# Performance work log

Measured on AMD Instinct MI355X. Metric: run time of the kernel, lower is better.

Reference implementation:

```python
import jax, jax.numpy as jnp
import numpy as np

B, S, D, H, FF, L, U = 64, 256, 128, 8, 512, 4, 5000
N, E, FEA, HW, CED, TD = 40000, 160000, 32, 16, 16, 6
DH = D // H


def _ln(x, g, b):
    m = jnp.mean(x, -1, keepdims=True)
    v = jnp.var(x, -1, keepdims=True)
    return (x - m) * jax.lax.rsqrt(v + 1e-5) * g + b


def _sin_pe(s, d):
    pos = jnp.arange(s, dtype=jnp.float32)[:, None]
    div = jnp.exp(jnp.arange(0, d, 2, dtype=jnp.float32) * (-np.log(10000.0) / d))
    ang = pos * div  # [S, D/2]
    return jnp.stack([jnp.sin(ang), jnp.cos(ang)], -1).reshape(s, d)


def setup_inputs() -> dict:
    key = jax.random.key(0)
    ks = jax.random.split(key, 40)
    sc = 0.02
    inp = {}
    inp['node_feature'] = jax.random.normal(ks[0], (N, FEA), jnp.float32)
    inp['edge_index'] = jax.random.randint(ks[1], (2, E), 0, N)
    inp['traj_x'] = jax.random.randint(ks[2], (B, S), 0, N)
    inp['temporal_x'] = jax.random.normal(ks[3], (B, S, TD), jnp.float32)
    inp['user_id_x'] = jax.random.randint(ks[4], (B, 1), 0, U)
    inp['mask'] = jnp.ones((B, S), jnp.int32)
    inp['end_idx'] = jax.random.randint(ks[5], (B,), 0, S)
    inp['idx_without_end'] = jax.random.randint(ks[6], (B,), 0, S)
    inp['temporal_mat_x'] = jax.random.uniform(ks[7], (B, S, S), jnp.float32) * 3600.0
    inp['dis_mat_x'] = jax.random.uniform(ks[8], (B, S, S), jnp.float32) * 5000.0
    inp['highway_x'] = jax.random.randint(ks[9], (B, S), 0, HW)
    inp['lambda2'] = jnp.float32(0.5)
    # --- learned parameters ---
    inp['gnn_w1'] = jax.random.normal(ks[10], (FEA, D), jnp.float32) * sc
    inp['gnn_b1'] = jnp.zeros((D,), jnp.float32)
    inp['gnn_w2'] = jax.random.normal(ks[11], (D, D), jnp.float32) * sc
    inp['gnn_b2'] = jnp.zeros((D,), jnp.float32)
    inp['ue_tab'] = jax.random.normal(ks[12], (U, D), jnp.float32) * sc
    inp['ce_tab'] = jax.random.normal(ks[13], (HW, CED), jnp.float32) * sc
    inp['fl_w'] = jax.random.normal(ks[14], (TD + CED, D), jnp.float32) * sc
    inp['fl_b'] = jnp.zeros((D,), jnp.float32)
    inp['wqkv'] = jax.random.normal(ks[15], (L, D, 3 * D), jnp.float32) * sc
    inp['bqkv'] = jnp.zeros((L, 3 * D), jnp.float32)
    inp['wo'] = jax.random.normal(ks[16], (L, D, D), jnp.float32) * sc
    inp['bo'] = jnp.zeros((L, D), jnp.float32)
    inp['ln1_g'] = jnp.ones((L, D), jnp.float32)
    inp['ln1_b'] = jnp.zeros((L, D), jnp.float32)
    inp['ln2_g'] = jnp.ones((L, D), jnp.float32)
    inp['ln2_b'] = jnp.zeros((L, D), jnp.float32)
    inp['ffn_w1'] = jax.random.normal(ks[17], (L, D, FF), jnp.float32) * sc
    inp['ffn_b1'] = jnp.zeros((L, FF), jnp.float32)
    inp['ffn_w2'] = jax.random.normal(ks[18], (L, FF, D), jnp.float32) * sc
    inp['ffn_b2'] = jnp.zeros((L, D), jnp.float32)
    inp['head_w'] = jax.random.normal(ks[19], (D, U), jnp.float32) * sc
    inp['head_b'] = jnp.zeros((U,), jnp.float32)
    return inp


def reference(node_feature, edge_index, traj_x, temporal_x, user_id_x, mask,
              end_idx, idx_without_end, temporal_mat_x, dis_mat_x, highway_x,
              lambda2,
              gnn_w1, gnn_b1, gnn_w2, gnn_b2, ue_tab, ce_tab, fl_w, fl_b,
              wqkv, bqkv, wo, bo, ln1_g, ln1_b, ln2_g, ln2_b,
              ffn_w1, ffn_b1, ffn_w2, ffn_b2, head_w, head_b):
    # --- spatial (road-network) GNN encoder: spe ---
    src, dst = edge_index[0], edge_index[1]
    deg = jax.ops.segment_sum(jnp.ones((E,), jnp.float32), dst, num_segments=N)
    h = node_feature
    for W, b in ((gnn_w1, gnn_b1), (gnn_w2, gnn_b2)):
        agg = jax.ops.segment_sum(h[src], dst, num_segments=N) / (deg[:, None] + 1.0)
        h = jax.nn.relu((h + agg) @ W + b)
    spe = h  # [N, D]
    # --- embedding fusion ---
    ce = ce_tab[highway_x]                                  # [B,S,CED]
    ue = ue_tab[user_id_x]                                  # [B,1,D] broadcast
    fuse = jax.nn.relu(jnp.concatenate([temporal_x, ce], -1) @ fl_w + fl_b)
    x = spe[traj_x] + ue + fuse                             # [B,S,D]
    x = x + _sin_pe(S, D)[None]
    # --- relative temporal/distance attention bias ---
    rel = lambda2 * jnp.log1p(temporal_mat_x) + (1.0 - lambda2) * jnp.log1p(dis_mat_x)
    mbias = jnp.where(mask[:, None, None, :] > 0, 0.0, -1e9)
    bias = mbias - rel[:, None]                             # [B,1,S,S]
    scale = 1.0 / float(np.sqrt(DH))
    for l in range(L):
        qkv = x @ wqkv[l] + bqkv[l]
        q, k, v = jnp.split(qkv, 3, axis=-1)
        q = q.reshape(B, S, H, DH).transpose(0, 2, 1, 3)
        k = k.reshape(B, S, H, DH).transpose(0, 2, 1, 3)
        v = v.reshape(B, S, H, DH).transpose(0, 2, 1, 3)
        scores = jnp.einsum('bhqd,bhkd->bhqk', q, k) * scale + bias
        a = jax.nn.softmax(scores, -1)
        o = jnp.einsum('bhqk,bhkd->bhqd', a, v).transpose(0, 2, 1, 3).reshape(B, S, D)
        x = _ln(x + o @ wo[l] + bo[l], ln1_g[l], ln1_b[l])
        f = jax.nn.relu(x @ ffn_w1[l] + ffn_b1[l]) @ ffn_w2[l] + ffn_b2[l]
        x = _ln(x + f, ln2_g[l], ln2_b[l])
    # --- gather last token + classifier head ---
    traj_emb = x[jnp.arange(B), end_idx]                    # [B,D]
    return traj_emb @ head_w + head_b                       # [B,U]
```

## Files before the change

kernel.cpp:

```cpp
#include <hip/hip_runtime.h>
#include <hip/hip_fp16.h>
#include <cstdint>
#include <cstddef>

typedef unsigned short u16;
typedef __attribute__((ext_vector_type(8))) short short8;
typedef __attribute__((ext_vector_type(4))) float f32x4;

#define B_   64
#define S_   256
#define D_   128
#define H_   8
#define DH_  16
#define FF_  512
#define L_   4
#define U_   5000
#define UP_  5120
#define N_   40000
#define NP_  40064
#define E_   160000
#define FEA_ 32
#define HWY_ 16
#define CED_ 16
#define TD_  6
#define NSCB 157
#define UB_CNT_END 160
#define UB_CVT_END 1592
#define UB_TOTAL   5688

static __device__ __forceinline__ u16 f2b(float f) {
    unsigned int u = __float_as_uint(f);
    unsigned int r = (u + 0x7FFFu + ((u >> 16) & 1u)) >> 16;
    return (u16)r;
}
static __device__ __forceinline__ float b2f(u16 u) {
    return __uint_as_float(((unsigned int)u) << 16);
}
static __device__ __forceinline__ u16 f2h(float f) {
    return __half_as_ushort(__float2half(f));
}
static __device__ __forceinline__ float h2f(u16 u) {
    return __half2float(__ushort_as_half(u));
}

static __device__ __forceinline__ void gload16(const void* g, void* l) {
    __builtin_amdgcn_global_load_lds(
        (const __attribute__((address_space(1))) unsigned int*)g,
        (__attribute__((address_space(3))) unsigned int*)l,
        16, 0, 0);
}

struct UberArgs {
    const float* csrc[7];
    u16* cdst[7];
    int K[7], Npad[7], Nsrc[7], Kp[7], base[7];
    const float* tm; const float* dm; const int* maskp; const float* lambda2;
    u16* bias; int* cnt;
};

__global__ __launch_bounds__(256) void k_uber(UberArgs a) {
    __shared__ float tile[32][33];
    int bid = blockIdx.x, tid = threadIdx.x;
    if (bid < UB_CNT_END) {
        int idx = bid * 256 + tid;
        if (idx < NP_) a.cnt[idx] = 0;
        return;
    }
    if (bid < UB_CVT_END) {
        int t = 0;
#pragma unroll
        for (int i = 1; i < 7; ++i) t += (bid >= a.base[i]);
        int rb = bid - a.base[t];
        int K = a.K[t], Npad = a.Npad[t], Nsrc = a.Nsrc[t], Kp = a.Kp[t];
        int nbn = Npad >> 5, nbk = Kp >> 5;
        int per = nbn * nbk;
        int l = rb / per, rem = rb - l * per;
        int n0 = (rem % nbn) * 32, k0 = (rem / nbn) * 32;
        const float* in = a.csrc[t];
        u16* outp = a.cdst[t];
        int j = tid & 31, i2 = tid >> 5;
#pragma unroll
        for (int r = 0; r < 4; ++r) {
            int k = k0 + i2 + r * 8, n = n0 + j;
            tile[i2 + r * 8][j] = (k < K && n < Nsrc) ? in[(size_t)l * K * Nsrc + (size_t)k * Nsrc + n] : 0.f;
        }
        __syncthreads();
#pragma unroll
        for (int r = 0; r < 4; ++r) {
            int n = n0 + i2 + r * 8, k = k0 + j;
            if (n < Npad && k < Kp)
                outp[(size_t)l * Npad * Kp + (size_t)n * Kp + k] = f2b(tile[j][i2 + r * 8]);
        }
        return;
    }
    int t4 = (bid - UB_CVT_END) * 256 + tid;
    const int total = B_ * S_ * S_ / 4;
    if (t4 >= total) return;
    float l2 = *a.lambda2, l2c = 1.f - l2;
    float4 av = ((const float4*)a.tm)[t4];
    float4 bv = ((const float4*)a.dm)[t4];
    int basei = t4 * 4;
    int bb = basei >> 16;
    int k0 = basei & 255;
    const int* mrow = a.maskp + bb * S_;
    float r0 = (mrow[k0 + 0] > 0 ? 0.f : -30000.f) - (l2 * __logf(1.f + av.x) + l2c * __logf(1.f + bv.x));
    float r1 = (mrow[k0 + 1] > 0 ? 0.f : -30000.f) - (l2 * __logf(1.f + av.y) + l2c * __logf(1.f + bv.y));
    float r2 = (mrow[k0 + 2] > 0 ? 0.f : -30000.f) - (l2 * __logf(1.f + av.z) + l2c * __logf(1.f + bv.z));
    float r3 = (mrow[k0 + 3] > 0 ? 0.f : -30000.f) - (l2 * __logf(1.f + av.w) + l2c * __logf(1.f + bv.w));
    *(ushort4*)&a.bias[(size_t)t4 * 4] = make_ushort4(f2h(r0), f2h(r1), f2h(r2), f2h(r3));
}

__global__ __launch_bounds__(256) void k_count(const int* __restrict__ dst, int* __restrict__ cnt) {
    int e = blockIdx.x * 256 + threadIdx.x;
    if (e < E_) atomicAdd(&cnt[dst[e]], 1);
}

__global__ __launch_bounds__(256) void k_scanA(const int* __restrict__ cnt, int* __restrict__ part) {
    __shared__ int sh[256];
    int idx = blockIdx.x * 256 + threadIdx.x;
    sh[threadIdx.x] = (idx < NP_) ? cnt[idx] : 0;
    __syncthreads();
    for (int o = 128; o > 0; o >>= 1) {
        if (threadIdx.x < o) sh[threadIdx.x] += sh[threadIdx.x + o];
        __syncthreads();
    }
    if (threadIdx.x == 0) part[blockIdx.x] = sh[0];
}

__global__ __launch_bounds__(256) void k_scanB(const int* __restrict__ cnt, const int* __restrict__ part,
                                               int* __restrict__ off, int* __restrict__ cursor) {
    __shared__ int sh[256];
    __shared__ int bsum;
    int tid = threadIdx.x;
    int pv = (tid < blockIdx.x) ? part[tid] : 0;
    sh[tid] = pv;
    __syncthreads();
    for (int o = 128; o > 0; o >>= 1) {
        if (tid < o) sh[tid] += sh[tid + o];
        __syncthreads();
    }
    if (tid == 0) bsum = sh[0];
    __syncthreads();
    int basev = bsum;
    __syncthreads();
    int idx = blockIdx.x * 256 + tid;
    int v = (idx < NP_) ? cnt[idx] : 0;
    sh[tid] = v;
    __syncthreads();
    for (int o = 1; o < 256; o <<= 1) {
        int t2 = (tid >= o) ? sh[tid - o] : 0;
        __syncthreads();
        sh[tid] += t2;
        __syncthreads();
    }
    if (idx < NP_) {
        int res = sh[tid] - v + basev;
        off[idx] = res;
        cursor[idx] = res;
    }
}

__global__ __launch_bounds__(256) void k_fill(const int* __restrict__ src, const int* __restrict__ dst,
                                              int* __restrict__ cursor, int* __restrict__ ebuf) {
    int e = blockIdx.x * 256 + threadIdx.x;
    if (e >= E_) return;
    int p = atomicAdd(&cursor[dst[e]], 1);
    ebuf[p] = src[e];
}

__global__ __launch_bounds__(256) void k_gprep1(const float* __restrict__ nf, const int* __restrict__ off,
                                                const int* __restrict__ cnt, const int* __restrict__ ebuf,
                                                u16* __restrict__ out) {
    int n = blockIdx.x * 8 + (threadIdx.x >> 5);
    int f = threadIdx.x & 31;
    u16 r = 0;
    if (n < N_) {
        int start = off[n], c = cnt[n];
        float acc = 0.f;
        int i = 0;
        for (; i + 4 <= c; i += 4) {
            int s0 = ebuf[start + i], s1 = ebuf[start + i + 1];
            int s2 = ebuf[start + i + 2], s3 = ebuf[start + i + 3];
            float v0 = nf[(size_t)s0 * FEA_ + f];
            float v1 = nf[(size_t)s1 * FEA_ + f];
            float v2 = nf[(size_t)s2 * FEA_ + f];
            float v3 = nf[(size_t)s3 * FEA_ + f];
            acc += (v0 + v1) + (v2 + v3);
        }
        for (; i < c; ++i) {
            int s = ebuf[start + i];
            acc += nf[(size_t)s * FEA_ + f];
        }
        r = f2b(nf[(size_t)n * FEA_ + f] + acc / (float)(c + 1));
    }
    if (n < NP_) {
        out[(size_t)n * 64 + f] = r;
        out[(size_t)n * 64 + 32 + f] = 0;
    }
}

__global__ __launch_bounds__(256) void k_gprep2(const u16* __restrict__ h1b, const int* __restrict__ off,
                                                const int* __restrict__ cnt, const int* __restrict__ ebuf,
                                                u16* __restrict__ out) {
    int n = blockIdx.x * 4 + (threadIdx.x >> 6);
    int d2 = (threadIdx.x & 63) * 2;
    if (n >= NP_) return;
    u16 r0 = 0, r1 = 0;
    if (n < N_) {
        int start = off[n], c = cnt[n];
        float a0 = 0.f, a1 = 0.f;
        int i = 0;
        for (; i + 4 <= c; i += 4) {
            int s0 = ebuf[start + i], s1 = ebuf[start + i + 1];
            int s2 = ebuf[start + i + 2], s3 = ebuf[start + i + 3];
            ushort2 v0 = *(const ushort2*)&h1b[(size_t)s0 * D_ + d2];
            ushort2 v1 = *(const ushort2*)&h1b[(size_t)s1 * D_ + d2];
            ushort2 v2 = *(const ushort2*)&h1b[(size_t)s2 * D_ + d2];
            ushort2 v3 = *(const ushort2*)&h1b[(size_t)s3 * D_ + d2];
            a0 += (b2f(v0.x) + b2f(v1.x)) + (b2f(v2.x) + b2f(v3.x));
            a1 += (b2f(v0.y) + b2f(v1.y)) + (b2f(v2.y) + b2f(v3.y));
        }
        for (; i < c; ++i) {
            int s = ebuf[start + i];
            ushort2 v = *(const ushort2*)&h1b[(size_t)s * D_ + d2];
            a0 += b2f(v.x); a1 += b2f(v.y);
        }
        float rinv = 1.f / (float)(c + 1);
        ushort2 sv = *(const ushort2*)&h1b[(size_t)n * D_ + d2];
        r0 = f2b(b2f(sv.x) + a0 * rinv);
        r1 = f2b(b2f(sv.y) + a1 * rinv);
    }
    *(ushort2*)&out[(size_t)n * D_ + d2] = make_ushort2(r0, r1);
}

template<int BM, int ACT, int OUTB, int RES, int LN, int GAT>
__global__ __launch_bounds__(256) void k_mgemm(const u16* __restrict__ A, const u16* __restrict__ BT,
                                               const float* __restrict__ bias, const float* __restrict__ resid,
                                               void* __restrict__ Cout,
                                               const float* __restrict__ g, const float* __restrict__ be,
                                               u16* __restrict__ xbout, const int* __restrict__ endi,
                                               int M, int N, int K) {
    constexpr int SMEMB = (BM == 128) ? (LN ? 128 * 133 * 4 : 32768)
                                      : (LN ? 64 * 133 * 4 : 24576);
    __shared__ __align__(16) char smem[SMEMB];
    u16* Al = (u16*)smem;
    u16* Bl = Al + (BM == 128 ? 128 * 64 : 64 * 64);
    int tid = threadIdx.x;
    int wid = tid >> 6, lane = tid & 63;
    int row0 = blockIdx.x * BM;
    int col0 = blockIdx.y * 128;
    f32x4 acc[4][4] = {};
    int rA = lane & 15, kq = lane >> 4;

    for (int k0 = 0; k0 < K; k0 += 64) {
        if (k0) __syncthreads();
        if (BM == 128) {
            int srow = wid * 32 + (lane >> 3);
            int ks8 = ((lane & 7) ^ (lane >> 3)) * 8;
#pragma unroll
            for (int i = 0; i < 4; ++i) {
                int row = srow + i * 8;
                size_t arow = (size_t)(row0 + row);
                if (GAT) {
                    int bb2 = row0 + row;
                    arow = (bb2 < B_) ? ((size_t)bb2 * S_ + endi[bb2]) : 0;
                }
                gload16(A + arow * K + k0 + ks8, &Al[(wid * 32 + i * 8) * 64]);
                gload16(BT + (size_t)(col0 + row) * K + k0 + ks8, &Bl[(wid * 32 + i * 8) * 64]);
            }
        } else {
#pragma unroll
            for (int i = 0; i < 6; ++i) {
                int c = wid * 6 + i;
                int rr = c * 8 + (lane >> 3);
                int sl = (((lane & 7) ^ (rr & 7)) << 3);
                if (c < 8) {
                    size_t arow = (size_t)(row0 + rr);
                    if (GAT) {
                        int bb2 = row0 + rr;
                        arow = (bb2 < B_) ? ((size_t)bb2 * S_ + endi[bb2]) : 0;
                    }
                    gload16(A + arow * K + k0 + sl, &Al[rr * 64]);
                } else {
                    gload16(BT + (size_t)(col0 + rr - 64) * K + k0 + sl, &Bl[(rr - 64) * 64]);
                }
            }
        }
        __syncthreads();
#pragma unroll
        for (int ks = 0; ks < 2; ++ks) {
            int sw = ((ks * 4 + kq) ^ (rA & 7)) * 8;
            if (BM == 128) {
                int wr = wid >> 1, wc = wid & 1;
                short8 af[4], bfr[4];
#pragma unroll
                for (int m = 0; m < 4; ++m)
                    af[m] = *(const short8*)&Al[(64 * wr + m * 16 + rA) * 64 + sw];
#pragma unroll
                for (int n = 0; n < 4; ++n)
                    bfr[n] = *(const short8*)&Bl[(64 * wc + n * 16 + rA) * 64 + sw];
#pragma unroll
                for (int m = 0; m < 4; ++m)
#pragma unroll
                    for (int n = 0; n < 4; ++n)
                        acc[m][n] = __builtin_amdgcn_mfma_f32_16x16x32_bf16(af[m], bfr[n], acc[m][n], 0, 0, 0);
            } else {
                int wr2 = wid & 1, wc2 = wid >> 1;
                short8 af[2], bfr[4];
#pragma unroll
                for (int m = 0; m < 2; ++m)
                    af[m] = *(const short8*)&Al[(wr2 * 32 + m * 16 + rA) * 64 + sw];
#pragma unroll
                for (int n = 0; n < 4; ++n)
                    bfr[n] = *(const short8*)&Bl[(wc2 * 64 + n * 16 + rA) * 64 + sw];
#pragma unroll
                for (int m = 0; m < 2; ++m)
#pragma unroll
                    for (int n = 0; n < 4; ++n)
                        acc[m][n] = __builtin_amdgcn_mfma_f32_16x16x32_bf16(af[m], bfr[n], acc[m][n], 0, 0, 0);
            }
        }
    }

    if (LN) {
        float* vbuf = (float*)smem;
        __syncthreads();
        constexpr int MR = (BM == 128) ? 4 : 2;
#pragma unroll
        for (int m = 0; m < MR; ++m) {
#pragma unroll
            for (int n = 0; n < 4; ++n) {
                int cc, rl0;
                if (BM == 128) { cc = (wid & 1) * 64 + n * 16 + rA; rl0 = (wid >> 1) * 64 + m * 16 + kq * 4; }
                else           { cc = (wid >> 1) * 64 + n * 16 + rA; rl0 = (wid & 1) * 32 + m * 16 + kq * 4; }
                float bv = bias[cc];
#pragma unroll
                for (int r = 0; r < 4; ++r) {
                    int rl = rl0 + r;
                    float v = acc[m][n][r] + bv + resid[(size_t)(row0 + rl) * 128 + cc];
                    vbuf[rl * 133 + cc] = v;
                }
            }
        }
        __syncthreads();
        if (BM == 128) {
            int rl = tid >> 1, half = tid & 1;
            const float* vrow = vbuf + rl * 133 + half * 64;
            float4 vv[16];
            float s = 0.f, s2 = 0.f;
#pragma unroll
            for (int j = 0; j < 16; ++j) {
                vv[j] = *(const float4*)(vrow + j * 4);
                s += (vv[j].x + vv[j].y) + (vv[j].z + vv[j].w);
                s2 += (vv[j].x * vv[j].x + vv[j].y * vv[j].y) + (vv[j].z * vv[j].z + vv[j].w * vv[j].w);
            }
            s += __shfl_xor(s, 1, 64);
            s2 += __shfl_xor(s2, 1, 64);
            float mean = s * (1.f / 128.f);
            float var = s2 * (1.f / 128.f) - mean * mean;
            float rs = rsqrtf(var + 1e-5f);
            int grow = row0 + rl;
            float* xrow = (float*)Cout + (size_t)grow * 128 + half * 64;
            u16* xbrow = xbout + (size_t)grow * 128 + half * 64;
#pragma unroll
            for (int j = 0; j < 16; ++j) {
                float4 gv = *(const float4*)(g + half * 64 + j * 4);
                float4 bv = *(const float4*)(be + half * 64 + j * 4);
                float o0 = (vv[j].x - mean) * rs * gv.x + bv.x;
                float o1 = (vv[j].y - mean) * rs * gv.y + bv.y;
                float o2 = (vv[j].z - mean) * rs * gv.z + bv.z;
                float o3 = (vv[j].w - mean) * rs * gv.w + bv.w;
                *(float4*)(xrow + j * 4) = make_float4(o0, o1, o2, o3);
                *(ushort4*)(xbrow + j * 4) = make_ushort4(f2b(o0), f2b(o1), f2b(o2), f2b(o3));
            }
        } else {
            int rl = tid >> 2, q4 = tid & 3;
            const float* vrow = vbuf + rl * 133 + q4 * 32;
            float4 vv[8];
            float s = 0.f, s2 = 0.f;
#pragma unroll
            for (int j = 0; j < 8; ++j) {
                vv[j] = *(const float4*)(vrow + j * 4);
                s += (vv[j].x + vv[j].y) + (vv[j].z + vv[j].w);
                s2 += (vv[j].x * vv[j].x + vv[j].y * vv[j].y) + (vv[j].z * vv[j].z + vv[j].w * vv[j].w);
            }
            s += __shfl_xor(s, 1, 64);  s2 += __shfl_xor(s2, 1, 64);
            s += __shfl_xor(s, 2, 64);  s2 += __shfl_xor(s2, 2, 64);
            float mean = s * (1.f / 128.f);
            float var = s2 * (1.f / 128.f) - mean * mean;
            float rs = rsqrtf(var + 1e-5f);
            int grow = row0 + rl;
            float* xrow = (float*)Cout + (size_t)grow * 128 + q4 * 32;
            u16* xbrow = xbout + (size_t)grow * 128 + q4 * 32;
#pragma unroll
            for (int j = 0; j < 8; ++j) {
                float4 gv = *(const float4*)(g + q4 * 32 + j * 4);
                float4 bv = *(const float4*)(be + q4 * 32 + j * 4);
                float o0 = (vv[j].x - mean) * rs * gv.x + bv.x;
                float o1 = (vv[j].y - mean) * rs * gv.y + bv.y;
                float o2 = (vv[j].z - mean) * rs * gv.z + bv.z;
                float o3 = (vv[j].w - mean) * rs * gv.w + bv.w;
                *(float4*)(xrow + j * 4) = make_float4(o0, o1, o2, o3);
                *(ushort4*)(xbrow + j * 4) = make_ushort4(f2b(o0), f2b(o1), f2b(o2), f2b(o3));
            }
        }
    } else {
        constexpr int MR = (BM == 128) ? 4 : 2;
#pragma unroll
        for (int m = 0; m < MR; ++m) {
#pragma unroll
            for (int n = 0; n < 4; ++n) {
                int cc, cr0;
                if (BM == 128) { cc = col0 + (wid & 1) * 64 + n * 16 + rA; cr0 = row0 + (wid >> 1) * 64 + m * 16 + kq * 4; }
                else           { cc = col0 + (wid >> 1) * 64 + n * 16 + rA; cr0 = row0 + (wid & 1) * 32 + m * 16 + kq * 4; }
                if (cc >= N) continue;
                float bv = bias[cc];
#pragma unroll
                for (int r = 0; r < 4; ++r) {
                    int cr = cr0 + r;
                    if (cr >= M) continue;
                    float v = acc[m][n][r] + bv;
                    if (RES) v += resid[(size_t)cr * N + cc];
                    if (ACT) v = fmaxf(v, 0.f);
                    if (OUTB) ((u16*)Cout)[(size_t)cr * N + cc] = f2b(v);
                    else      ((float*)Cout)[(size_t)cr * N + cc] = v;
                }
            }
        }
    }
}

#define KLS 40
#define VTS 272
__global__ __launch_bounds__(256) void k_qkvatt(const u16* __restrict__ xb, const u16* __restrict__ wT,
                                                const float* __restrict__ bq, const u16* __restrict__ bias,
                                                u16* __restrict__ o) {
    __shared__ __align__(16) char smem[73728];
    u16* Kl  = (u16*)smem;
    u16* Vt  = (u16*)(smem + 20480);
    u16* Ql  = (u16*)(smem + 29184);
    u16* Pl  = (u16*)(smem + 37376);
    u16* Ast = (u16*)smem;
    u16* Bst = (u16*)(smem + 32768);
    int idx = blockIdx.x;
    int b = (idx & 7) * 8 + (idx >> 6);
    int h = (idx >> 3) & 7;
    int tid = threadIdx.x, wid = tid >> 6, lane = tid & 63;
    int rA = lane & 15, kq = lane >> 4;

    f32x4 acc[4][3] = {};
    for (int k0 = 0; k0 < 128; k0 += 64) {
        if (k0) __syncthreads();
#pragma unroll
        for (int i = 0; i < 8; ++i) {
            int row = wid * 64 + i * 8 + (lane >> 3);
            int sl = (((lane & 7) ^ (row & 7)) << 3);
            gload16(xb + ((size_t)(b * S_ + row)) * 128 + k0 + sl, &Ast[(wid * 64 + i * 8) * 64]);
        }
        if (wid < 3) {
#pragma unroll
            for (int i = 0; i < 2; ++i) {
                int c = wid * 2 + i;
                int brow = c * 8 + (lane >> 3);
                int grow = wid * 128 + h * 16 + (brow & 15);
                int sl = (((lane & 7) ^ (brow & 7)) << 3);
                gload16(wT + (size_t)grow * 128 + k0 + sl, &Bst[c * 8 * 64]);
            }
        }
        __syncthreads();
#pragma unroll
        for (int ks = 0; ks < 2; ++ks) {
            int sw = ((ks * 4 + kq) ^ (rA & 7)) * 8;
            short8 af[4], bfr[3];
#pragma unroll
            for (int m = 0; m < 4; ++m)
                af[m] = *(const short8*)&Ast[(wid * 64 + m * 16 + rA) * 64 + sw];
#pragma unroll
            for (int n = 0; n < 3; ++n)
                bfr[n] = *(const short8*)&Bst[(n * 16 + rA) * 64 + sw];
#pragma unroll
            for (int m = 0; m < 4; ++m)
#pragma unroll
                for (int n = 0; n < 3; ++n)
                    acc[m][n] = __builtin_amdgcn_mfma_f32_16x16x32_bf16(af[m], bfr[n], acc[m][n], 0, 0, 0);
        }
    }
    __syncthreads();
    {
        short8 z = {};
        *(short8*)&Kl[tid * KLS + 16] = z;
        *(short8*)&Kl[tid * KLS + 24] = z;
    }
    {
        float bq0 = bq[h * 16 + rA];
        float bq1 = bq[128 + h * 16 + rA];
        float bq2 = bq[256 + h * 16 + rA];
#pragma unroll
        for (int m = 0; m < 4; ++m) {
            int cr0 = wid * 64 + m * 16 + kq * 4;
#pragma unroll
            for (int r = 0; r < 4; ++r) {
                int row = cr0 + r;
                Ql[row * 16 + rA]  = f2b(acc[m][0][r] + bq0);
                Kl[row * KLS + rA] = f2b(acc[m][1][r] + bq1);
                Vt[rA * VTS + row] = f2b(acc[m][2][r] + bq2);
            }
        }
    }
    __syncthreads();

    u16* pl = Pl + wid * 16 * VTS;
    int qi = lane & 15;
    for (int qt = 0; qt < 4; ++qt) {
        int q = wid * 64 + qt * 16 + qi;
        ushort4 bb[16];
        const u16* bp = bias + (size_t)b * (S_ * S_) + (size_t)q * S_ + kq * 4;
#pragma unroll
        for (int t = 0; t < 16; ++t) bb[t] = *(const ushort4*)(bp + t * 16);
        short8 qf = {};
        if (lane < 32)
            qf = *(const short8*)&Ql[q * 16 + kq * 8];
        f32x4 sc[16];
#pragma unroll
        for (int t = 0; t < 16; ++t) {
            short8 kf = *(const short8*)&Kl[(t * 16 + qi) * KLS + kq * 8];
            f32x4 zz = {0.f, 0.f, 0.f, 0.f};
            sc[t] = __builtin_amdgcn_mfma_f32_16x16x32_bf16(kf, qf, zz, 0, 0, 0);
        }
        float m = -1e30f;
#pragma unroll
        for (int t = 0; t < 16; ++t) {
            sc[t][0] = sc[t][0] * 0.25f + h2f(bb[t].x);
            sc[t][1] = sc[t][1] * 0.25f + h2f(bb[t].y);
            sc[t][2] = sc[t][2] * 0.25f + h2f(bb[t].z);
            sc[t][3] = sc[t][3] * 0.25f + h2f(bb[t].w);
            m = fmaxf(m, fmaxf(fmaxf(sc[t][0], sc[t][1]), fmaxf(sc[t][2], sc[t][3])));
        }
        m = fmaxf(m, __shfl_xor(m, 16, 64));
        m = fmaxf(m, __shfl_xor(m, 32, 64));
        float l = 0.f;
#pragma unroll
        for (int t = 0; t < 16; ++t) {
            sc[t][0] = __expf(sc[t][0] - m);
            sc[t][1] = __expf(sc[t][1] - m);
            sc[t][2] = __expf(sc[t][2] - m);
            sc[t][3] = __expf(sc[t][3] - m);
            l += (sc[t][0] + sc[t][1]) + (sc[t][2] + sc[t][3]);
        }
        l += __shfl_xor(l, 16, 64);
        l += __shfl_xor(l, 32, 64);
        float inv = 1.f / l;
#pragma unroll
        for (int t = 0; t < 16; ++t) {
            ushort4 pw = make_ushort4(f2b(sc[t][0] * inv), f2b(sc[t][1] * inv),
                                      f2b(sc[t][2] * inv), f2b(sc[t][3] * inv));
            *(ushort4*)&pl[qi * VTS + t * 16 + kq * 4] = pw;
        }
        f32x4 oa = {0.f, 0.f, 0.f, 0.f};
#pragma unroll
        for (int w8 = 0; w8 < 8; ++w8) {
            short8 vf = *(const short8*)&Vt[qi * VTS + w8 * 32 + kq * 8];
            short8 pf = *(const short8*)&pl[qi * VTS + w8 * 32 + kq * 8];
            oa = __builtin_amdgcn_mfma_f32_16x16x32_bf16(vf, pf, oa, 0, 0, 0);
        }
        ushort4 ow = make_ushort4(f2b(oa[0]), f2b(oa[1]), f2b(oa[2]), f2b(oa[3]));
        *(ushort4*)&o[((size_t)(b * S_ + q)) * D_ + h * 16 + kq * 4] = ow;
    }
}

__global__ __launch_bounds__(256) void k_ffn(const u16* __restrict__ xbin,
                                             const u16* __restrict__ w1T, const float* __restrict__ b1,
                                             const u16* __restrict__ w2T, const float* __restrict__ b2,
                                             const float* __restrict__ g, const float* __restrict__ be,
                                             float* __restrict__ x, u16* __restrict__ xbout) {
    __shared__ __align__(16) char smem[73728];
    u16* Alds = (u16*)smem;
    u16* Wlds = (u16*)(smem + 8192);
    u16* f1   = (u16*)(smem + 40960);
    float* vbuf = (float*)smem;
    int tid = threadIdx.x, wid = tid >> 6, lane = tid & 63;
    int rows0 = blockIdx.x * 32;
    int rA = lane & 15, kq = lane >> 4;

#pragma unroll
    for (int j = 0; j < 2; ++j) {
        int row = wid * 8 + j * 4 + (lane >> 4);
        int win = (lane >> 3) & 1, slot = lane & 7;
        gload16(xbin + (size_t)(rows0 + row) * 128 + win * 64 + ((slot ^ (row & 7)) << 3),
                Alds + (wid * 8 + j * 4) * 128);
    }

    for (int nh = 0; nh < 2; ++nh) {
        f32x4 acc1[2][4] = {};
        for (int k0 = 0; k0 < 128; k0 += 64) {
            __syncthreads();
#pragma unroll
            for (int i = 0; i < 8; ++i) {
                int rl2 = i * 32 + wid * 8 + (lane >> 3);
                gload16(w1T + (size_t)(nh * 256 + rl2) * 128 + k0 + (((lane & 7) ^ (rl2 & 7)) << 3),
                        Wlds + (i * 32 + wid * 8) * 64);
            }
            __syncthreads();
#pragma unroll
            for (int ks = 0; ks < 2; ++ks) {
                int sw = ((ks * 4 + kq) ^ (rA & 7)) << 3;
                short8 af[2], bf4[4];
                af[0] = *(const short8*)&Alds[rA * 128 + k0 + sw];
                af[1] = *(const short8*)&Alds[(16 + rA) * 128 + k0 + sw];
#pragma unroll
                for (int n = 0; n < 4; ++n)
                    bf4[n] = *(const short8*)&Wlds[(wid * 64 + n * 16 + rA) * 64 + sw];
#pragma unroll
                for (int m = 0; m < 2; ++m)
#pragma unroll
                    for (int n = 0; n < 4; ++n)
                        acc1[m][n] = __builtin_amdgcn_mfma_f32_16x16x32_bf16(af[m], bf4[n], acc1[m][n], 0, 0, 0);
            }
        }
#pragma unroll
        for (int m = 0; m < 2; ++m)
#pragma unroll
            for (int n = 0; n < 4; ++n) {
                int cc = nh * 256 + wid * 64 + n * 16 + rA;
                float bv = b1[cc];
#pragma unroll
                for (int r = 0; r < 4; ++r) {
                    int rl = m * 16 + kq * 4 + r;
                    float v = fmaxf(acc1[m][n][r] + bv, 0.f);
                    int scol = (cc & ~63) | (((((cc >> 3) & 7) ^ (rl & 7)) & 7) << 3) | (cc & 7);
                    f1[rl * 512 + scol] = f2b(v);
                }
            }
    }
    __syncthreads();

    f32x4 acc2[2][2] = {};
    for (int k0 = 0; k0 < 512; k0 += 64) {
        if (k0) __syncthreads();
#pragma unroll
        for (int i = 0; i < 4; ++i) {
            int rl2 = i * 32 + wid * 8 + (lane >> 3);
            gload16(w2T + (size_t)rl2 * 512 + k0 + (((lane & 7) ^ (rl2 & 7)) << 3),
                    Wlds + (i * 32 + wid * 8) * 64);
        }
        __syncthreads();
#pragma unroll
        for (int ks = 0; ks < 2; ++ks) {
            int sw = ((ks * 4 + kq) ^ (rA & 7)) << 3;
            short8 af0 = *(const short8*)&f1[rA * 512 + k0 + sw];
            short8 af1 = *(const short8*)&f1[(16 + rA) * 512 + k0 + sw];
            short8 bf0 = *(const short8*)&Wlds[(wid * 32 + rA) * 64 + sw];
            short8 bf1 = *(const short8*)&Wlds[(wid * 32 + 16 + rA) * 64 + sw];
            acc2[0][0] = __builtin_amdgcn_mfma_f32_16x16x32_bf16(af0, bf0, acc2[0][0], 0, 0, 0);
            acc2[0][1] = __builtin_amdgcn_mfma_f32_16x16x32_bf16(af0, bf1, acc2[0][1], 0, 0, 0);
            acc2[1][0] = __builtin_amdgcn_mfma_f32_16x16x32_bf16(af1, bf0, acc2[1][0], 0, 0, 0);
            acc2[1][1] = __builtin_amdgcn_mfma_f32_16x16x32_bf16(af1, bf1, acc2[1][1], 0, 0, 0);
        }
    }

    __syncthreads();
#pragma unroll
    for (int m = 0; m < 2; ++m)
#pragma unroll
        for (int n = 0; n < 2; ++n) {
            int cc = wid * 32 + n * 16 + rA;
            float bv = b2[cc];
#pragma unroll
            for (int r = 0; r < 4; ++r) {
                int rl = m * 16 + kq * 4 + r;
                float v = acc2[m][n][r] + bv + x[(size_t)(rows0 + rl) * 128 + cc];
                vbuf[rl * 133 + cc] = v;
            }
        }
    __syncthreads();
    int row = tid >> 3, sub = tid & 7;
    const float* vr = vbuf + row * 133 + sub * 16;
    float vv[16];
    float s = 0.f, s2 = 0.f;
#pragma unroll
    for (int j = 0; j < 16; ++j) {
        vv[j] = vr[j];
        s += vv[j];
        s2 += vv[j] * vv[j];
    }
    s += __shfl_xor(s, 1, 64);  s2 += __shfl_xor(s2, 1, 64);
    s += __shfl_xor(s, 2, 64);  s2 += __shfl_xor(s2, 2, 64);
    s += __shfl_xor(s, 4, 64);  s2 += __shfl_xor(s2, 4, 64);
    float mean = s * (1.f / 128.f);
    float var = s2 * (1.f / 128.f) - mean * mean;
    float rs = rsqrtf(var + 1e-5f);
    int grow = rows0 + row;
    float* xrow = x + (size_t)grow * 128 + sub * 16;
    u16* xbrow = xbout + (size_t)grow * 128 + sub * 16;
#pragma unroll
    for (int j = 0; j < 4; ++j) {
        float4 gv = *(const float4*)(g + sub * 16 + j * 4);
        float4 bv = *(const float4*)(be + sub * 16 + j * 4);
        float o0 = (vv[j * 4 + 0] - mean) * rs * gv.x + bv.x;
        float o1 = (vv[j * 4 + 1] - mean) * rs * gv.y + bv.y;
        float o2 = (vv[j * 4 + 2] - mean) * rs * gv.z + bv.z;
        float o3 = (vv[j * 4 + 3] - mean) * rs * gv.w + bv.w;
        *(float4*)(xrow + j * 4) = make_float4(o0, o1, o2, o3);
        *(ushort4*)(xbrow + j * 4) = make_ushort4(f2b(o0), f2b(o1), f2b(o2), f2b(o3));
    }
}

__global__ __launch_bounds__(256) void k_fusion(const float* __restrict__ spe, const int* __restrict__ traj,
                                                const float* __restrict__ ue_tab, const int* __restrict__ uid,
                                                const float* __restrict__ tempx, const int* __restrict__ hwx,
                                                const float* __restrict__ ce_tab, const float* __restrict__ flw,
                                                const float* __restrict__ flb, float* __restrict__ x,
                                                u16* __restrict__ xb) {
    __shared__ float Ws[22 * D_];
    __shared__ float bs[D_];
    __shared__ float ins[2][22];
    int tid = threadIdx.x;
    for (int i = tid; i < 22 * D_; i += 256) Ws[i] = flw[i];
    if (tid < D_) bs[tid] = flb[tid];
    __syncthreads();
    int ro = tid >> 7, d = tid & 127;
    int base = blockIdx.x * 32;
    for (int ir = 0; ir < 16; ++ir) {
        int tok = base + ir * 2 + ro;
        int b = tok >> 8, s = tok & 255;
        if (d < TD_) ins[ro][d] = tempx[(size_t)tok * TD_ + d];
        else if (d < 22) ins[ro][d] = ce_tab[(size_t)hwx[tok] * CED_ + (d - TD_)];
        __syncthreads();
        float acc = bs[d];
#pragma unroll
        for (int k = 0; k < 22; ++k) acc = fmaf(ins[ro][k], Ws[k * D_ + d], acc);
        acc = fmaxf(acc, 0.f);
        int i2 = d & ~1;
        float ang = (float)s * __expf(-(float)i2 * 0.0719557841560639f);
        float pe = (d & 1) ? cosf(ang) : sinf(ang);
        float v = spe[(size_t)traj[tok] * D_ + d] + ue_tab[(size_t)uid[b] * D_ + d] + acc + pe;
        x[(size_t)tok * D_ + d] = v;
        xb[(size_t)tok * D_ + d] = f2b(v);
        __syncthreads();
    }
}

extern "C" void kernel_launch(void* const* d_in, const int* in_sizes, int n_in,
                              void* d_out, int out_size, void* d_ws, size_t ws_size,
                              hipStream_t stream) {
    const float* node_feature = (const float*)d_in[0];
    const int*   edge_index   = (const int*)d_in[1];
    const int*   traj_x       = (const int*)d_in[2];
    const float* temporal_x   = (const float*)d_in[3];
    const int*   user_id_x    = (const int*)d_in[4];
    const int*   mask         = (const int*)d_in[5];
    const int*   end_idx      = (const int*)d_in[6];
    const float* tmat         = (const float*)d_in[8];
    const float* dmat         = (const float*)d_in[9];
    const int*   highway_x    = (const int*)d_in[10];
    const float* lambda2      = (const float*)d_in[11];
    const float* gnn_w1       = (const float*)d_in[12];
    const float* gnn_b1       = (const float*)d_in[13];
    const float* gnn_w2       = (const float*)d_in[14];
    const float* gnn_b2       = (const float*)d_in[15];
    const float* ue_tab       = (const float*)d_in[16];
    const float* ce_tab       = (const float*)d_in[17];
    const float* fl_w         = (const float*)d_in[18];
    const float* fl_b         = (const float*)d_in[19];
    const float* wqkv         = (const float*)d_in[20];
    const float* bqkv         = (const float*)d_in[21];
    const float* wo           = (const float*)d_in[22];
    const float* bo           = (const float*)d_in[23];
    const float* ln1_g        = (const float*)d_in[24];
    const float* ln1_b        = (const float*)d_in[25];
    const float* ln2_g        = (const float*)d_in[26];
    const float* ln2_b        = (const float*)d_in[27];
    const float* ffn_w1       = (const float*)d_in[28];
    const float* ffn_b1       = (const float*)d_in[29];
    const float* ffn_w2       = (const float*)d_in[30];
    const float* ffn_b2       = (const float*)d_in[31];
    const float* head_w       = (const float*)d_in[32];
    const float* head_b       = (const float*)d_in[33];
    float* out = (float*)d_out;

    float* w     = (float*)d_ws;
    int*   cnt   = (int*)w;
    float* spe   = w + 40960;
    u16*   biasb = (u16*)(w + 5169152);
    float* wreg  = w + 7266304;
    u16* wqkvT = (u16*)wreg;
    u16* woT   = wqkvT + 4 * 384 * 128;
    u16* w1T   = woT + 4 * 128 * 128;
    u16* w2T   = w1T + 4 * 512 * 128;
    u16* gw1T  = w2T + 4 * 128 * 512;
    u16* gw2T  = gw1T + 128 * 64;
    u16* hwT   = gw2T + 128 * 128;
    float* pool  = w + 8000000;
    u16*   h1b   = (u16*)pool;
    u16*   in1b  = (u16*)(pool + 2564096);
    u16*   in2b  = (u16*)(pool + 3846144);
    int*   off   = (int*)(pool + 6410240);
    int*   cursor= (int*)(pool + 6450304);
    int*   ebuf  = (int*)(pool + 6490368);
    int*   part  = (int*)(pool + 6650368);
    float* x     = pool;
    u16*   xb    = (u16*)(pool + 2097152);
    u16*   attob = (u16*)(pool + 4718592);

    const int* esrc = edge_index;
    const int* edst = edge_index + E_;

    UberArgs ua;
    const float* srcs[7] = {wqkv, wo, ffn_w1, ffn_w2, gnn_w1, gnn_w2, head_w};
    u16* dsts[7]        = {wqkvT, woT, w1T, w2T, gw1T, gw2T, hwT};
    int Ks[7]    = {128, 128, 128, 512, 32, 128, 128};
    int Npads[7] = {384, 128, 512, 128, 128, 128, UP_};
    int Nsrcs[7] = {384, 128, 512, 128, 128, 128, U_};
    int Kps[7]   = {128, 128, 128, 512, 64, 128, 128};
    int Ls[7]    = {4, 4, 4, 4, 1, 1, 1};
    int bb = UB_CNT_END;
    for (int t = 0; t < 7; ++t) {
        ua.csrc[t] = srcs[t]; ua.cdst[t] = dsts[t];
        ua.K[t] = Ks[t]; ua.Npad[t] = Npads[t]; ua.Nsrc[t] = Nsrcs[t]; ua.Kp[t] = Kps[t];
        ua.base[t] = bb;
        bb += (Npads[t] / 32) * (Kps[t] / 32) * Ls[t];
    }
    ua.tm = tmat; ua.dm = dmat; ua.maskp = mask; ua.lambda2 = lambda2;
    ua.bias = biasb; ua.cnt = cnt;
    k_uber<<<UB_TOTAL, 256, 0, stream>>>(ua);

    k_count<<<(E_ + 255) / 256, 256, 0, stream>>>(edst, cnt);
    k_scanA<<<NSCB, 256, 0, stream>>>(cnt, part);
    k_scanB<<<NSCB, 256, 0, stream>>>(cnt, part, off, cursor);
    k_fill<<<(E_ + 255) / 256, 256, 0, stream>>>(esrc, edst, cursor, ebuf);
    k_gprep1<<<NP_ / 8, 256, 0, stream>>>(node_feature, off, cnt, ebuf, in1b);
    k_mgemm<128, 1, 1, 0, 0, 0><<<dim3(NP_ / 128, 1), 256, 0, stream>>>(in1b, gw1T, gnn_b1, nullptr, h1b,
                                                                        nullptr, nullptr, nullptr, nullptr, NP_, D_, 64);
    k_gprep2<<<NP_ / 4, 256, 0, stream>>>(h1b, off, cnt, ebuf, in2b);
    k_mgemm<128, 1, 0, 0, 0, 0><<<dim3(NP_ / 128, 1), 256, 0, stream>>>(in2b, gw2T, gnn_b2, nullptr, spe,
                                                                        nullptr, nullptr, nullptr, nullptr, NP_, D_, D_);

    k_fusion<<<(B_ * S_) / 32, 256, 0, stream>>>(spe, traj_x, ue_tab, user_id_x,
                                                 temporal_x, highway_x, ce_tab, fl_w, fl_b, x, xb);

    const int M = B_ * S_;
    for (int l = 0; l < L_; ++l) {
        k_qkvatt<<<B_ * H_, 256, 0, stream>>>(xb, wqkvT + (size_t)l * 384 * 128,
                                              bqkv + (size_t)l * 384, biasb, attob);
        k_mgemm<64, 0, 0, 1, 1, 0><<<dim3(M / 64, 1), 256, 0, stream>>>(attob, woT + (size_t)l * 128 * 128,
                                                                        bo + l * D_, x, x,
                                                                        ln1_g + l * D_, ln1_b + l * D_, xb, nullptr, M, D_, D_);
        k_ffn<<<M / 32, 256, 0, stream>>>(xb, w1T + (size_t)l * 512 * 128, ffn_b1 + l * FF_,
                                          w2T + (size_t)l * 128 * 512, ffn_b2 + l * D_,
                                          ln2_g + l * D_, ln2_b + l * D_, x, xb);
    }

    k_mgemm<64, 0, 0, 0, 0, 1><<<dim3(1, UP_ / 128), 256, 0, stream>>>(xb, hwT, head_b, nullptr, out,
                                                                       nullptr, nullptr, nullptr, end_idx, B_, U_, D_);
}
```

Measured before the change: 350.3 us.

## Fuse output projection and first LayerNorm into the FFN kernel

The per-layer Wo projection with residual add and LayerNorm moves into the FFN kernel as a new k_layer, so each 32-row tile computes attention-out projection, LN1, FFN and LN2 in one launch. The LN1 result stays in registers and LDS as the FFN input and second residual, so the round trip of x and xb through global memory between the two kernels goes away. The generic GEMM loses its residual and LN variants. Each block now reloads the full Wo weight, and the kernel carries more registers, which may lower occupancy.

```diff
diff --git a/kernel.cpp b/kernel.cpp
--- a/kernel.cpp
+++ b/kernel.cpp
@@ -233,15 +233,11 @@
     *(ushort2*)&out[(size_t)n * D_ + d2] = make_ushort2(r0, r1);
 }
 
-template<int BM, int ACT, int OUTB, int RES, int LN, int GAT>
+template<int BM, int ACT, int OUTB, int GAT>
 __global__ __launch_bounds__(256) void k_mgemm(const u16* __restrict__ A, const u16* __restrict__ BT,
-                                               const float* __restrict__ bias, const float* __restrict__ resid,
-                                               void* __restrict__ Cout,
-                                               const float* __restrict__ g, const float* __restrict__ be,
-                                               u16* __restrict__ xbout, const int* __restrict__ endi,
-                                               int M, int N, int K) {
-    constexpr int SMEMB = (BM == 128) ? (LN ? 128 * 133 * 4 : 32768)
-                                      : (LN ? 64 * 133 * 4 : 24576);
+                                               const float* __restrict__ bias, void* __restrict__ Cout,
+                                               const int* __restrict__ endi, int M, int N, int K) {
+    constexpr int SMEMB = (BM == 128) ? 32768 : 24576;
     __shared__ __align__(16) char smem[SMEMB];
     u16* Al = (u16*)smem;
     u16* Bl = Al + (BM == 128 ? 128 * 64 : 64 * 64);
@@ -322,109 +318,24 @@
         }
     }
 
-    if (LN) {
-        float* vbuf = (float*)smem;
-        __syncthreads();
-        constexpr int MR = (BM == 128) ? 4 : 2;
-#pragma unroll
-        for (int m = 0; m < MR; ++m) {
-#pragma unroll
-            for (int n = 0; n < 4; ++n) {
-                int cc, rl0;
-                if (BM == 128) { cc = (wid & 1) * 64 + n * 16 + rA; rl0 = (wid >> 1) * 64 + m * 16 + kq * 4; }
-                else           { cc = (wid >> 1) * 64 + n * 16 + rA; rl0 = (wid & 1) * 32 + m * 16 + kq * 4; }
-                float bv = bias[cc];
-#pragma unroll
-                for (int r = 0; r < 4; ++r) {
-                    int rl = rl0 + r;
-                    float v = acc[m][n][r] + bv + resid[(size_t)(row0 + rl) * 128 + cc];
-                    vbuf[rl * 133 + cc] = v;
-                }
-            }
-        }
-        __syncthreads();
-        if (BM == 128) {
-            int rl = tid >> 1, half = tid & 1;
-            const float* vrow = vbuf + rl * 133 + half * 64;
-            float4 vv[16];
-            float s = 0.f, s2 = 0.f;
-#pragma unroll
-            for (int j = 0; j < 16; ++j) {
-                vv[j] = *(const float4*)(vrow + j * 4);
-                s += (vv[j].x + vv[j].y) + (vv[j].z + vv[j].w);
-                s2 += (vv[j].x * vv[j].x + vv[j].y * vv[j].y) + (vv[j].z * vv[j].z + vv[j].w * vv[j].w);
-            }
-            s += __shfl_xor(s, 1, 64);
-            s2 += __shfl_xor(s2, 1, 64);
-            float mean = s * (1.f / 128.f);
-            float var = s2 * (1.f / 128.f) - mean * mean;
-            float rs = rsqrtf(var + 1e-5f);
-            int grow = row0 + rl;
-            float* xrow = (float*)Cout + (size_t)grow * 128 + half * 64;
-            u16* xbrow = xbout + (size_t)grow * 128 + half * 64;
-#pragma unroll
-            for (int j = 0; j < 16; ++j) {
-                float4 gv = *(const float4*)(g + half * 64 + j * 4);
-                float4 bv = *(const float4*)(be + half * 64 + j * 4);
-                float o0 = (vv[j].x - mean) * rs * gv.x + bv.x;
-                float o1 = (vv[j].y - mean) * rs * gv.y + bv.y;
-                float o2 = (vv[j].z - mean) * rs * gv.z + bv.z;
-                float o3 = (vv[j].w - mean) * rs * gv.w + bv.w;
-                *(float4*)(xrow + j * 4) = make_float4(o0, o1, o2, o3);
-                *(ushort4*)(xbrow + j * 4) = make_ushort4(f2b(o0), f2b(o1), f2b(o2), f2b(o3));
-            }
-        } else {
-            int rl = tid >> 2, q4 = tid & 3;
-            const float* vrow = vbuf + rl * 133 + q4 * 32;
-            float4 vv[8];
-            float s = 0.f, s2 = 0.f;
-#pragma unroll
-            for (int j = 0; j < 8; ++j) {
-                vv[j] = *(const float4*)(vrow + j * 4);
-                s += (vv[j].x + vv[j].y) + (vv[j].z + vv[j].w);
-                s2 += (vv[j].x * vv[j].x + vv[j].y * vv[j].y) + (vv[j].z * vv[j].z + vv[j].w * vv[j].w);
-            }
-            s += __shfl_xor(s, 1, 64);  s2 += __shfl_xor(s2, 1, 64);
-            s += __shfl_xor(s, 2, 64);  s2 += __shfl_xor(s2, 2, 64);
-            float mean = s * (1.f / 128.f);
-            float var = s2 * (1.f / 128.f) - mean * mean;
-            float rs = rsqrtf(var + 1e-5f);
-            int grow = row0 + rl;
-            float* xrow = (float*)Cout + (size_t)grow * 128 + q4 * 32;
-            u16* xbrow = xbout + (size_t)grow * 128 + q4 * 32;
-#pragma unroll
-            for (int j = 0; j < 8; ++j) {
-                float4 gv = *(const float4*)(g + q4 * 32 + j * 4);
-                float4 bv = *(const float4*)(be + q4 * 32 + j * 4);
-                float o0 = (vv[j].x - mean) * rs * gv.x + bv.x;
-                float o1 = (vv[j].y - mean) * rs * gv.y + bv.y;
-                float o2 = (vv[j].z - mean) * rs * gv.z + bv.z;
-                float o3 = (vv[j].w - mean) * rs * gv.w + bv.w;
-                *(float4*)(xrow + j * 4) = make_float4(o0, o1, o2, o3);
-                *(ushort4*)(xbrow + j * 4) = make_ushort4(f2b(o0), f2b(o1), f2b(o2), f2b(o3));
-            }
-        }
-    } else {
-        constexpr int MR = (BM == 128) ? 4 : 2;
-#pragma unroll
-        for (int m = 0; m < MR; ++m) {
-#pragma unroll
-            for (int n = 0; n < 4; ++n) {
-                int cc, cr0;
-                if (BM == 128) { cc = col0 + (wid & 1) * 64 + n * 16 + rA; cr0 = row0 + (wid >> 1) * 64 + m * 16 + kq * 4; }
-                else           { cc = col0 + (wid >> 1) * 64 + n * 16 + rA; cr0 = row0 + (wid & 1) * 32 + m * 16 + kq * 4; }
-                if (cc >= N) continue;
-                float bv = bias[cc];
-#pragma unroll
-                for (int r = 0; r < 4; ++r) {
-                    int cr = cr0 + r;
-                    if (cr >= M) continue;
-                    float v = acc[m][n][r] + bv;
-                    if (RES) v += resid[(size_t)cr * N + cc];
-                    if (ACT) v = fmaxf(v, 0.f);
-                    if (OUTB) ((u16*)Cout)[(size_t)cr * N + cc] = f2b(v);
-                    else      ((float*)Cout)[(size_t)cr * N + cc] = v;
-                }
+    constexpr int MR = (BM == 128) ? 4 : 2;
+#pragma unroll
+    for (int m = 0; m < MR; ++m) {
+#pragma unroll
+        for (int n = 0; n < 4; ++n) {
+            int cc, cr0;
+            if (BM == 128) { cc = col0 + (wid & 1) * 64 + n * 16 + rA; cr0 = row0 + (wid >> 1) * 64 + m * 16 + kq * 4; }
+            else           { cc = col0 + (wid >> 1) * 64 + n * 16 + rA; cr0 = row0 + (wid & 1) * 32 + m * 16 + kq * 4; }
+            if (cc >= N) continue;
+            float bv = bias[cc];
+#pragma unroll
+            for (int r = 0; r < 4; ++r) {
+                int cr = cr0 + r;
+                if (cr >= M) continue;
+                float v = acc[m][n][r] + bv;
+                if (ACT) v = fmaxf(v, 0.f);
+                if (OUTB) ((u16*)Cout)[(size_t)cr * N + cc] = f2b(v);
+                else      ((float*)Cout)[(size_t)cr * N + cc] = v;
             }
         }
     }
@@ -568,11 +479,13 @@
     }
 }
 
-__global__ __launch_bounds__(256) void k_ffn(const u16* __restrict__ xbin,
-                                             const u16* __restrict__ w1T, const float* __restrict__ b1,
-                                             const u16* __restrict__ w2T, const float* __restrict__ b2,
-                                             const float* __restrict__ g, const float* __restrict__ be,
-                                             float* __restrict__ x, u16* __restrict__ xbout) {
+__global__ __launch_bounds__(256) void k_layer(const u16* __restrict__ atto,
+                                               const u16* __restrict__ woT, const float* __restrict__ bo,
+                                               const float* __restrict__ ln1g, const float* __restrict__ ln1b,
+                                               const u16* __restrict__ w1T, const float* __restrict__ b1,
+                                               const u16* __restrict__ w2T, const float* __restrict__ b2,
+                                               const float* __restrict__ ln2g, const float* __restrict__ ln2b,
+                                               float* __restrict__ x, u16* __restrict__ xbout) {
     __shared__ __align__(16) char smem[73728];
     u16* Alds = (u16*)smem;
     u16* Wlds = (u16*)(smem + 8192);
@@ -581,13 +494,86 @@
     int tid = threadIdx.x, wid = tid >> 6, lane = tid & 63;
     int rows0 = blockIdx.x * 32;
     int rA = lane & 15, kq = lane >> 4;
+    int row = tid >> 3, sub = tid & 7;
 
 #pragma unroll
     for (int j = 0; j < 2; ++j) {
-        int row = wid * 8 + j * 4 + (lane >> 4);
+        int srow = wid * 8 + j * 4 + (lane >> 4);
         int win = (lane >> 3) & 1, slot = lane & 7;
-        gload16(xbin + (size_t)(rows0 + row) * 128 + win * 64 + ((slot ^ (row & 7)) << 3),
+        gload16(atto + (size_t)(rows0 + srow) * 128 + win * 64 + ((slot ^ (srow & 7)) << 3),
                 Alds + (wid * 8 + j * 4) * 128);
+    }
+
+    f32x4 accw[2][2] = {};
+    for (int k0 = 0; k0 < 128; k0 += 64) {
+        __syncthreads();
+#pragma unroll
+        for (int i = 0; i < 4; ++i) {
+            int rl2 = i * 32 + wid * 8 + (lane >> 3);
+            gload16(woT + (size_t)rl2 * 128 + k0 + (((lane & 7) ^ (rl2 & 7)) << 3),
+                    Wlds + (i * 32 + wid * 8) * 64);
+        }
+        __syncthreads();
+#pragma unroll
+        for (int ks = 0; ks < 2; ++ks) {
+            int sw = ((ks * 4 + kq) ^ (rA & 7)) << 3;
+            short8 af0 = *(const short8*)&Alds[rA * 128 + k0 + sw];
+            short8 af1 = *(const short8*)&Alds[(16 + rA) * 128 + k0 + sw];
+            short8 bf0 = *(const short8*)&Wlds[(wid * 32 + rA) * 64 + sw];
+            short8 bf1 = *(const short8*)&Wlds[(wid * 32 + 16 + rA) * 64 + sw];
+            accw[0][0] = __builtin_amdgcn_mfma_f32_16x16x32_bf16(af0, bf0, accw[0][0], 0, 0, 0);
+            accw[0][1] = __builtin_amdgcn_mfma_f32_16x16x32_bf16(af0, bf1, accw[0][1], 0, 0, 0);
+            accw[1][0] = __builtin_amdgcn_mfma_f32_16x16x32_bf16(af1, bf0, accw[1][0], 0, 0, 0);
+            accw[1][1] = __builtin_amdgcn_mfma_f32_16x16x32_bf16(af1, bf1, accw[1][1], 0, 0, 0);
+        }
+    }
+
+    __syncthreads();
+#pragma unroll
+    for (int m = 0; m < 2; ++m)
+#pragma unroll
+        for (int n = 0; n < 2; ++n) {
+            int cc = wid * 32 + n * 16 + rA;
+            float bv = bo[cc];
+#pragma unroll
+            for (int r = 0; r < 4; ++r) {
+                int rl = m * 16 + kq * 4 + r;
+                vbuf[rl * 133 + cc] = accw[m][n][r] + bv + x[(size_t)(rows0 + rl) * 128 + cc];
+            }
+        }
+    __syncthreads();
+    float x1[16];
+    {
+        const float* vr = vbuf + row * 133 + sub * 16;
+        float s = 0.f, s2 = 0.f;
+#pragma unroll
+        for (int j = 0; j < 16; ++j) {
+            x1[j] = vr[j];
+            s += x1[j];
+            s2 += x1[j] * x1[j];
+        }
+        s += __shfl_xor(s, 1, 64);  s2 += __shfl_xor(s2, 1, 64);
+        s += __shfl_xor(s, 2, 64);  s2 += __shfl_xor(s2, 2, 64);
+        s += __shfl_xor(s, 4, 64);  s2 += __shfl_xor(s2, 4, 64);
+        float mean = s * (1.f / 128.f);
+        float var = s2 * (1.f / 128.f) - mean * mean;
+        float rs = rsqrtf(var + 1e-5f);
+#pragma unroll
+        for (int j = 0; j < 4; ++j) {
+            float4 gv = *(const float4*)(ln1g + sub * 16 + j * 4);
+            float4 bv = *(const float4*)(ln1b + sub * 16 + j * 4);
+            x1[j * 4 + 0] = (x1[j * 4 + 0] - mean) * rs * gv.x + bv.x;
+            x1[j * 4 + 1] = (x1[j * 4 + 1] - mean) * rs * gv.y + bv.y;
+            x1[j * 4 + 2] = (x1[j * 4 + 2] - mean) * rs * gv.z + bv.z;
+            x1[j * 4 + 3] = (x1[j * 4 + 3] - mean) * rs * gv.w + bv.w;
+        }
+    }
+    __syncthreads();
+#pragma unroll
+    for (int j = 0; j < 16; ++j) {
+        int c = sub * 16 + j;
+        int sc = (c & ~63) | ((((c >> 3) & 7) ^ (row & 7)) << 3) | (c & 7);
+        Alds[row * 128 + sc] = f2b(x1[j]);
     }
 
     for (int nh = 0; nh < 2; ++nh) {
@@ -668,40 +654,40 @@
 #pragma unroll
             for (int r = 0; r < 4; ++r) {
                 int rl = m * 16 + kq * 4 + r;
-                float v = acc2[m][n][r] + bv + x[(size_t)(rows0 + rl) * 128 + cc];
-                vbuf[rl * 133 + cc] = v;
-            }
-        }
-    __syncthreads();
-    int row = tid >> 3, sub = tid & 7;
-    const float* vr = vbuf + row * 133 + sub * 16;
-    float vv[16];
-    float s = 0.f, s2 = 0.f;
-#pragma unroll
-    for (int j = 0; j < 16; ++j) {
-        vv[j] = vr[j];
-        s += vv[j];
-        s2 += vv[j] * vv[j];
-    }
-    s += __shfl_xor(s, 1, 64);  s2 += __shfl_xor(s2, 1, 64);
-    s += __shfl_xor(s, 2, 64);  s2 += __shfl_xor(s2, 2, 64);
-    s += __shfl_xor(s, 4, 64);  s2 += __shfl_xor(s2, 4, 64);
-    float mean = s * (1.f / 128.f);
-    float var = s2 * (1.f / 128.f) - mean * mean;
-    float rs = rsqrtf(var + 1e-5f);
-    int grow = rows0 + row;
-    float* xrow = x + (size_t)grow * 128 + sub * 16;
-    u16* xbrow = xbout + (size_t)grow * 128 + sub * 16;
-#pragma unroll
-    for (int j = 0; j < 4; ++j) {
-        float4 gv = *(const float4*)(g + sub * 16 + j * 4);
-        float4 bv = *(const float4*)(be + sub * 16 + j * 4);
-        float o0 = (vv[j * 4 + 0] - mean) * rs * gv.x + bv.x;
-        float o1 = (vv[j * 4 + 1] - mean) * rs * gv.y + bv.y;
-        float o2 = (vv[j * 4 + 2] - mean) * rs * gv.z + bv.z;
-        float o3 = (vv[j * 4 + 3] - mean) * rs * gv.w + bv.w;
-        *(float4*)(xrow + j * 4) = make_float4(o0, o1, o2, o3);
-        *(ushort4*)(xbrow + j * 4) = make_ushort4(f2b(o0), f2b(o1), f2b(o2), f2b(o3));
+                vbuf[rl * 133 + cc] = acc2[m][n][r] + bv;
+            }
+        }
+    __syncthreads();
+    {
+        const float* vr = vbuf + row * 133 + sub * 16;
+        float vv[16];
+        float s = 0.f, s2 = 0.f;
+#pragma unroll
+        for (int j = 0; j < 16; ++j) {
+            vv[j] = vr[j] + x1[j];
+            s += vv[j];
+            s2 += vv[j] * vv[j];
+        }
+        s += __shfl_xor(s, 1, 64);  s2 += __shfl_xor(s2, 1, 64);
+        s += __shfl_xor(s, 2, 64);  s2 += __shfl_xor(s2, 2, 64);
+        s += __shfl_xor(s, 4, 64);  s2 += __shfl_xor(s2, 4, 64);
+        float mean = s * (1.f / 128.f);
+        float var = s2 * (1.f / 128.f) - mean * mean;
+        float rs = rsqrtf(var + 1e-5f);
+        int grow = rows0 + row;
+        float* xrow = x + (size_t)grow * 128 + sub * 16;
+        u16* xbrow = xbout + (size_t)grow * 128 + sub * 16;
+#pragma unroll
+        for (int j = 0; j < 4; ++j) {
+            float4 gv = *(const float4*)(ln2g + sub * 16 + j * 4);
+            float4 bv = *(const float4*)(ln2b + sub * 16 + j * 4);
+            float o0 = (vv[j * 4 + 0] - mean) * rs * gv.x + bv.x;
+            float o1 = (vv[j * 4 + 1] - mean) * rs * gv.y + bv.y;
+            float o2 = (vv[j * 4 + 2] - mean) * rs * gv.z + bv.z;
+            float o3 = (vv[j * 4 + 3] - mean) * rs * gv.w + bv.w;
+            *(float4*)(xrow + j * 4) = make_float4(o0, o1, o2, o3);
+            *(ushort4*)(xbrow + j * 4) = make_ushort4(f2b(o0), f2b(o1), f2b(o2), f2b(o3));
+        }
     }
 }
 
@@ -829,11 +815,9 @@
     k_scanB<<<NSCB, 256, 0, stream>>>(cnt, part, off, cursor);
     k_fill<<<(E_ + 255) / 256, 256, 0, stream>>>(esrc, edst, cursor, ebuf);
     k_gprep1<<<NP_ / 8, 256, 0, stream>>>(node_feature, off, cnt, ebuf, in1b);
-    k_mgemm<128, 1, 1, 0, 0, 0><<<dim3(NP_ / 128, 1), 256, 0, stream>>>(in1b, gw1T, gnn_b1, nullptr, h1b,
-                                                                        nullptr, nullptr, nullptr, nullptr, NP_, D_, 64);
+    k_mgemm<128, 1, 1, 0><<<dim3(NP_ / 128, 1), 256, 0, stream>>>(in1b, gw1T, gnn_b1, h1b, nullptr, NP_, D_, 64);
     k_gprep2<<<NP_ / 4, 256, 0, stream>>>(h1b, off, cnt, ebuf, in2b);
-    k_mgemm<128, 1, 0, 0, 0, 0><<<dim3(NP_ / 128, 1), 256, 0, stream>>>(in2b, gw2T, gnn_b2, nullptr, spe,
-                                                                        nullptr, nullptr, nullptr, nullptr, NP_, D_, D_);
+    k_mgemm<128, 1, 0, 0><<<dim3(NP_ / 128, 1), 256, 0, stream>>>(in2b, gw2T, gnn_b2, spe, nullptr, NP_, D_, D_);
 
     k_fusion<<<(B_ * S_) / 32, 256, 0, stream>>>(spe, traj_x, ue_tab, user_id_x,
                                                  temporal_x, highway_x, ce_tab, fl_w, fl_b, x, xb);
@@ -842,14 +826,12 @@
     for (int l = 0; l < L_; ++l) {
         k_qkvatt<<<B_ * H_, 256, 0, stream>>>(xb, wqkvT + (size_t)l * 384 * 128,
                                               bqkv + (size_t)l * 384, biasb, attob);
-        k_mgemm<64, 0, 0, 1, 1, 0><<<dim3(M / 64, 1), 256, 0, stream>>>(attob, woT + (size_t)l * 128 * 128,
-                                                                        bo + l * D_, x, x,
-                                                                        ln1_g + l * D_, ln1_b + l * D_, xb, nullptr, M, D_, D_);
-        k_ffn<<<M / 32, 256, 0, stream>>>(xb, w1T + (size_t)l * 512 * 128, ffn_b1 + l * FF_,
-                                          w2T + (size_t)l * 128 * 512, ffn_b2 + l * D_,
-                                          ln2_g + l * D_, ln2_b + l * D_, x, xb);
-    }
-
-    k_mgemm<64, 0, 0, 0, 0, 1><<<dim3(1, UP_ / 128), 256, 0, stream>>>(xb, hwT, head_b, nullptr, out,
-                                                                       nullptr, nullptr, nullptr, end_idx, B_, U_, D_);
-}
+        k_layer<<<M / 32, 256, 0, stream>>>(attob, woT + (size_t)l * 128 * 128, bo + l * D_,
+                                            ln1_g + l * D_, ln1_b + l * D_,
+                                            w1T + (size_t)l * 512 * 128, ffn_b1 + l * FF_,
+                                            w2T + (size_t)l * 128 * 512, ffn_b2 + l * D_,
+                                            ln2_g + l * D_, ln2_b + l * D_, x, xb);
+    }
+
+    k_mgemm<64, 0, 0, 1><<<dim3(1, UP_ / 128), 256, 0, stream>>>(xb, hwT, head_b, out, end_idx, B_, U_, D_);
+}
```

After: 303.2 us. 1.16x faster.
